# Kernel optimization log

Measured on AMD Instinct MI355X. Metric: run time of the kernel, lower is better.

Reference implementation:

```python
import jax, jax.numpy as jnp
import numpy as np

B, N, F, H = 2, 2048, 1024, 16
D = F // H  # head_dim = 64
SCALE = D ** -0.5


def setup_inputs() -> dict:
    key = jax.random.key(0)
    ks = jax.random.split(key, 5)
    std = F ** -0.5
    return {
        "x": jax.random.normal(ks[0], (B, N, F), dtype=jnp.float32),
        "Wq": jax.random.normal(ks[1], (F, F), dtype=jnp.float32) * std,
        "Wk": jax.random.normal(ks[2], (F, F), dtype=jnp.float32) * std,
        "Wv": jax.random.normal(ks[3], (F, F), dtype=jnp.float32) * std,
        "Wo": jax.random.normal(ks[4], (F, F), dtype=jnp.float32) * std,
        "bo": jnp.zeros((F,), dtype=jnp.float32),
    }


def reference(x, Wq, Wk, Wv, Wo, bo):
    b, n, f = x.shape
    # nn.Linear computes x @ W.T
    q = (x @ Wq.T).reshape(b, n, H, D).transpose(0, 2, 1, 3)  # bhnd
    k = (x @ Wk.T).reshape(b, n, H, D).transpose(0, 2, 1, 3)
    v = (x @ Wv.T).reshape(b, n, H, D).transpose(0, 2, 1, 3)
    score = jax.nn.softmax(jnp.einsum('bhif,bhjf->bhij', q, k) * SCALE, axis=-1)
    attn = jnp.einsum('bhij,bhjf->bihf', score, v)  # (b, n, h, d)
    o = attn.reshape(b, n, f) @ Wo.T + bo
    return o
```

## Files before the change

kernel.cpp:

```cpp
#include <hip/hip_runtime.h>
#include <hip/hip_bf16.h>

#define B_    2
#define NSEQ  2048
#define FDIM  1024
#define NH    16
#define HD    64
#define MTOT  (B_*NSEQ)
#define BHSZ  (NSEQ*HD)

typedef __bf16 bf16_t;
typedef __bf16 bf16x4 __attribute__((ext_vector_type(4)));
typedef __bf16 bf16x8 __attribute__((ext_vector_type(8)));
typedef float  f32x4  __attribute__((ext_vector_type(4)));

#define AS1 __attribute__((address_space(1)))
#define AS3 __attribute__((address_space(3)))

#if __has_builtin(__builtin_amdgcn_exp2f)
#define EXP2(x) __builtin_amdgcn_exp2f(x)
#else
#define EXP2(x) exp2f(x)
#endif

__device__ __forceinline__ void gld_lds16(const bf16_t* g, bf16_t* l) {
  __builtin_amdgcn_global_load_lds((const AS1 void*)g, (AS3 void*)l, 16, 0, 0);
}

extern "C" __global__ __launch_bounds__(256) void cast_all_k(
    const float* __restrict__ x,  const float* __restrict__ wq,
    const float* __restrict__ wk, const float* __restrict__ wv,
    const float* __restrict__ wo,
    bf16_t* __restrict__ xb,  bf16_t* __restrict__ wqb,
    bf16_t* __restrict__ wkb, bf16_t* __restrict__ wvb,
    bf16_t* __restrict__ wob)
{
  long t = (long)blockIdx.x * blockDim.x + threadIdx.x;
  long i = t * 4;
  const float* src; bf16_t* dst; long off;
  if      (i < 4194304L) { src = x;  dst = xb;  off = i; }
  else if (i < 5242880L) { src = wq; dst = wqb; off = i - 4194304L; }
  else if (i < 6291456L) { src = wk; dst = wkb; off = i - 5242880L; }
  else if (i < 7340032L) { src = wv; dst = wvb; off = i - 6291456L; }
  else                   { src = wo; dst = wob; off = i - 7340032L; }
  float4 v = *(const float4*)(src + off);
  bf16x4 o = { (bf16_t)v.x, (bf16_t)v.y, (bf16_t)v.z, (bf16_t)v.w };
  *(bf16x4*)(dst + off) = o;
}

extern "C" __global__ __launch_bounds__(512) void gemm_bt_k(
    const bf16_t* __restrict__ A,
    const bf16_t* __restrict__ Bq, const bf16_t* __restrict__ Bk,
    const bf16_t* __restrict__ Bv,
    bf16_t* __restrict__ oq, bf16_t* __restrict__ okk,
    bf16_t* __restrict__ ovt)
{
  __shared__ __align__(16) char garena[33792];
  bf16_t* As = (bf16_t*)garena;
  bf16_t* Bs = (bf16_t*)(garena + 16384);
  const int K = FDIM;
  int mode = blockIdx.z;
  const bf16_t* Bw = (mode == 0) ? Bq : (mode == 1) ? Bk : Bv;
  int m0 = blockIdx.x * 128, n0 = blockIdx.y * 128;
  int tid = threadIdx.x, lane = tid & 63, wave = tid >> 6;
  int g = lane >> 4, c = lane & 15;
  int wm = (wave & 1) * 64, wn = (wave >> 1) * 32;
  f32x4 acc[4][2];
  for (int i = 0; i < 4; ++i)
    for (int j = 0; j < 2; ++j)
      acc[i][j] = (f32x4){0.f, 0.f, 0.f, 0.f};

  int srow = lane >> 2;
  int scol = (lane & 3) * 8;

  for (int kt = 0; kt < K / 64; ++kt) {
    int kk = kt * 64;
    {
      int chunk = wave;
      const bf16_t* ag = A  + (long)(m0 + chunk*16 + srow) * K + kk + scol;
      const bf16_t* bg = Bw + (long)(n0 + chunk*16 + srow) * K + kk + scol;
      gld_lds16(ag,      As + chunk * 512);
      gld_lds16(ag + 32, As + 4096 + chunk * 512);
      gld_lds16(bg,      Bs + chunk * 512);
      gld_lds16(bg + 32, Bs + 4096 + chunk * 512);
    }
    __syncthreads();
    bf16x8 af[4][2], bfr[2][2];
    for (int t = 0; t < 4; ++t) {
      af[t][0]  = *(const bf16x8*)(As + (wm + t*16 + c) * 32 + g * 8);
      af[t][1]  = *(const bf16x8*)(As + 4096 + (wm + t*16 + c) * 32 + g * 8);
    }
    for (int t = 0; t < 2; ++t) {
      bfr[t][0] = *(const bf16x8*)(Bs + (wn + t*16 + c) * 32 + g * 8);
      bfr[t][1] = *(const bf16x8*)(Bs + 4096 + (wn + t*16 + c) * 32 + g * 8);
    }
    for (int mt = 0; mt < 4; ++mt)
      for (int nt = 0; nt < 2; ++nt) {
        acc[mt][nt] = __builtin_amdgcn_mfma_f32_16x16x32_bf16(
            af[mt][0], bfr[nt][0], acc[mt][nt], 0, 0, 0);
        acc[mt][nt] = __builtin_amdgcn_mfma_f32_16x16x32_bf16(
            af[mt][1], bfr[nt][1], acc[mt][nt], 0, 0, 0);
      }
    __syncthreads();
  }

  bf16_t* Tl = (bf16_t*)garena;
  float sc = (mode == 0) ? 0.18033688011112042f : 1.0f;
  if (mode < 2) {
    for (int mt = 0; mt < 4; ++mt)
      for (int nt = 0; nt < 2; ++nt) {
        int nloc = wn + nt*16 + c;
        for (int r = 0; r < 4; ++r) {
          int mloc = wm + mt*16 + g*4 + r;
          Tl[mloc*132 + nloc] = (bf16_t)(acc[mt][nt][r] * sc);
        }
      }
  } else {
    for (int mt = 0; mt < 4; ++mt)
      for (int nt = 0; nt < 2; ++nt) {
        int nloc = wn + nt*16 + c;
        int mloc = wm + mt*16 + g*4;
        bf16x4 pk = { (bf16_t)acc[mt][nt][0], (bf16_t)acc[mt][nt][1],
                      (bf16_t)acc[mt][nt][2], (bf16_t)acc[mt][nt][3] };
        *(bf16x4*)(Tl + nloc*132 + mloc) = pk;
      }
  }
  __syncthreads();

  int b = m0 >> 11, m0loc = m0 & 2047;
  int h0 = n0 >> 6, tile0 = m0loc >> 6;
  int hoff = (mode == 2) ? 16 : 4;
#pragma unroll
  for (int u = 0; u < 4; ++u) {
    int chunk = u * 512 + tid;
    bf16_t* dst;
    int sidx;
    if (mode == 0) {
      int headloc = chunk >> 10, o = chunk & 1023;
      int tokloc = o >> 3, dd = (o & 7) * 8;
      sidx = tokloc*132 + headloc*64 + dd;
      dst = oq + ((long)(b*NH + h0 + headloc) * NSEQ + m0loc) * HD + (long)o * 8;
    } else if (mode == 1) {
      int region = chunk >> 9, o = chunk & 511;
      int headloc = region >> 1, t = region & 1;
      int f = o >> 6, rest = o & 63;
      int mtA = f >> 1, kh = f & 1, gK = rest >> 4, cA = rest & 15;
      int tokloc = t*64 + mtA*16 + cA;
      sidx = tokloc*132 + headloc*64 + kh*32 + gK*8;
      dst = okk + (long)(b*NH + h0 + headloc) * BHSZ
            + (long)(tile0 + t) * 4096 + (long)o * 8;
    } else {
      int region = chunk >> 9, o = chunk & 511;
      int headloc = region >> 1, t = region & 1;
      int c2 = o >> 8, dt = (o >> 6) & 3, ln = o & 63;
      int gA = ln >> 4, cA = ln & 15;
      sidx = (headloc*64 + dt*16 + cA) * 132 + t*64 + c2*32 + gA*4;
      dst = ovt + (long)(b*NH + h0 + headloc) * BHSZ
            + (long)(tile0 + t) * 4096 + (long)o * 8;
    }
    bf16x4 lo = *(const bf16x4*)(Tl + sidx);
    bf16x4 hi = *(const bf16x4*)(Tl + sidx + hoff);
    bf16x8 v;
#pragma unroll
    for (int i = 0; i < 4; ++i) { v[i] = lo[i]; v[i+4] = hi[i]; }
    *(bf16x8*)dst = v;
  }
}

extern "C" __global__ __launch_bounds__(512) void gemm_out_k(
    const bf16_t* __restrict__ A, const bf16_t* __restrict__ W,
    const float* __restrict__ bias, float* __restrict__ out)
{
  __shared__ __align__(16) bf16_t As[8192];
  __shared__ __align__(16) bf16_t Bs[4096];
  const int K = FDIM;
  int m0 = blockIdx.x * 128, n0 = blockIdx.y * 64;
  int tid = threadIdx.x, lane = tid & 63, wave = tid >> 6;
  int g = lane >> 4, c = lane & 15;
  int wm = (wave & 3) * 32, wn = (wave >> 2) * 32;
  f32x4 acc[2][2];
  for (int i = 0; i < 2; ++i)
    for (int j = 0; j < 2; ++j)
      acc[i][j] = (f32x4){0.f, 0.f, 0.f, 0.f};

  int srow = lane >> 2;
  int scol = (lane & 3) * 8;

  for (int kt = 0; kt < K / 64; ++kt) {
    int kk = kt * 64;
    {
      const bf16_t* ag = A + (long)(m0 + wave*16 + srow) * K + kk + scol;
      gld_lds16(ag,      As + wave * 512);
      gld_lds16(ag + 32, As + 4096 + wave * 512);
      if (wave < 4) {
        const bf16_t* bg = W + (long)(n0 + wave*16 + srow) * K + kk + scol;
        gld_lds16(bg,      Bs + wave * 512);
        gld_lds16(bg + 32, Bs + 2048 + wave * 512);
      }
    }
    __syncthreads();
    bf16x8 af[2][2], bfr[2][2];
    for (int t = 0; t < 2; ++t) {
      af[t][0]  = *(const bf16x8*)(As + (wm + t*16 + c) * 32 + g * 8);
      af[t][1]  = *(const bf16x8*)(As + 4096 + (wm + t*16 + c) * 32 + g * 8);
      bfr[t][0] = *(const bf16x8*)(Bs + (wn + t*16 + c) * 32 + g * 8);
      bfr[t][1] = *(const bf16x8*)(Bs + 2048 + (wn + t*16 + c) * 32 + g * 8);
    }
    for (int mt = 0; mt < 2; ++mt)
      for (int nt = 0; nt < 2; ++nt) {
        acc[mt][nt] = __builtin_amdgcn_mfma_f32_16x16x32_bf16(
            af[mt][0], bfr[nt][0], acc[mt][nt], 0, 0, 0);
        acc[mt][nt] = __builtin_amdgcn_mfma_f32_16x16x32_bf16(
            af[mt][1], bfr[nt][1], acc[mt][nt], 0, 0, 0);
      }
    __syncthreads();
  }

  for (int mt = 0; mt < 2; ++mt)
    for (int nt = 0; nt < 2; ++nt) {
      int n = n0 + wn + nt*16 + c;
      float bv = bias[n];
      for (int r = 0; r < 4; ++r) {
        int m = m0 + wm + mt*16 + g*4 + r;
        out[(long)m * FDIM + n] = acc[mt][nt][r] + bv;
      }
    }
}

extern "C" __global__ __launch_bounds__(512) void attn_fused_k(
    const bf16_t* __restrict__ q, const bf16_t* __restrict__ k,
    const bf16_t* __restrict__ vt, bf16_t* __restrict__ attn)
{
  __shared__ __align__(16) char arena[65536];
  __shared__ float Ll[128];
  int bh = blockIdx.y;
  int tid = threadIdx.x, lane = tid & 63, wave = tid >> 6;
  int g = lane >> 4, c = lane & 15;
  int qg = wave & 3, half = wave >> 2;
  int qw = blockIdx.x * 128 + qg * 32;
  const bf16_t* Q  = q  + (long)bh * NSEQ * HD;
  const bf16_t* Kf = k  + (long)bh * BHSZ;
  const bf16_t* Vf = vt + (long)bh * BHSZ;

  bf16x8 bQ[2][2];
#pragma unroll
  for (int s = 0; s < 2; ++s)
#pragma unroll
    for (int hh = 0; hh < 2; ++hh)
      bQ[s][hh] = *(const bf16x8*)(Q + (long)(qw + s*16 + c) * HD + hh*32 + g*8);

  f32x4 acc[2][4];
  f32x4 accl[2];
#pragma unroll
  for (int s = 0; s < 2; ++s) {
#pragma unroll
    for (int dt = 0; dt < 4; ++dt) acc[s][dt] = (f32x4){0.f, 0.f, 0.f, 0.f};
    accl[s] = (f32x4){0.f, 0.f, 0.f, 0.f};
  }

  bf16x8 ones;
#pragma unroll
  for (int i = 0; i < 8; ++i) ones[i] = (bf16_t)1.0f;

  int w4 = wave & 3, ln = lane;
  const int NT = NSEQ / 128;
  int kbase = half * (NSEQ / 2);

  auto stage = [&](int buf, int k0) {
    bf16_t* Kb = (bf16_t*)(arena + buf * 32768 + half * 16384);
    bf16_t* Vb = Kb + 4096;
    long tbase = (long)(k0 >> 6) * 4096;
#pragma unroll
    for (int j = 0; j < 2; ++j) {
      int ch = j*4 + w4;
      gld_lds16(Kf + tbase + ch*512 + ln*8, Kb + ch*512);
      gld_lds16(Vf + tbase + ch*512 + ln*8, Vb + ch*512);
    }
  };

  stage(0, kbase);
  __syncthreads();

  for (int kt = 0; kt < NT; ++kt) {
    int cur = kt & 1;
    if (kt + 1 < NT) stage(cur ^ 1, kbase + (kt + 1) * 64);

    const bf16_t* Kb = (const bf16_t*)(arena + cur * 32768 + half * 16384);
    const bf16_t* Vb = Kb + 4096;

    f32x4 St[2][4];
    __builtin_amdgcn_s_setprio(1);
#pragma unroll
    for (int mt = 0; mt < 4; ++mt) {
      bf16x8 k0f = *(const bf16x8*)(Kb + (mt*2 + 0) * 512 + lane * 8);
      bf16x8 k1f = *(const bf16x8*)(Kb + (mt*2 + 1) * 512 + lane * 8);
#pragma unroll
      for (int s = 0; s < 2; ++s) {
        f32x4 z = (f32x4){0.f, 0.f, 0.f, 0.f};
        z = __builtin_amdgcn_mfma_f32_16x16x32_bf16(k0f, bQ[s][0], z, 0, 0, 0);
        z = __builtin_amdgcn_mfma_f32_16x16x32_bf16(k1f, bQ[s][1], z, 0, 0, 0);
        St[s][mt] = z;
      }
    }
    __builtin_amdgcn_s_setprio(0);

    bf16x8 bP[2][2];
#pragma unroll
    for (int s = 0; s < 2; ++s)
#pragma unroll
      for (int c2 = 0; c2 < 2; ++c2) {
        f32x4 pa = St[s][c2*2 + 0];
        f32x4 pb = St[s][c2*2 + 1];
        bf16x8 t;
#pragma unroll
        for (int r = 0; r < 4; ++r) {
          t[r]     = (bf16_t)EXP2(pa[r]);
          t[r + 4] = (bf16_t)EXP2(pb[r]);
        }
        bP[s][c2] = t;
      }

    __builtin_amdgcn_s_setprio(1);
#pragma unroll
    for (int c2 = 0; c2 < 2; ++c2) {
      accl[0] = __builtin_amdgcn_mfma_f32_16x16x32_bf16(ones, bP[0][c2], accl[0], 0, 0, 0);
      accl[1] = __builtin_amdgcn_mfma_f32_16x16x32_bf16(ones, bP[1][c2], accl[1], 0, 0, 0);
#pragma unroll
      for (int dt = 0; dt < 4; ++dt) {
        bf16x8 aV = *(const bf16x8*)(Vb + (c2*4 + dt) * 512 + lane * 8);
        acc[0][dt] = __builtin_amdgcn_mfma_f32_16x16x32_bf16(
            aV, bP[0][c2], acc[0][dt], 0, 0, 0);
        acc[1][dt] = __builtin_amdgcn_mfma_f32_16x16x32_bf16(
            aV, bP[1][c2], acc[1][dt], 0, 0, 0);
      }
    }
    __builtin_amdgcn_s_setprio(0);

    __syncthreads();
  }

  float lp[2];
#pragma unroll
  for (int s = 0; s < 2; ++s) lp[s] = accl[s][0];

  float* Opart = (float*)arena;
  bf16_t* Tb = (bf16_t*)(arena + 36864);
  if (half == 1) {
#pragma unroll
    for (int s = 0; s < 2; ++s) {
      int qrow = qg*32 + s*16 + c;
#pragma unroll
      for (int dt = 0; dt < 4; ++dt)
        *(f32x4*)(Opart + qrow*72 + dt*16 + g*4) = acc[s][dt];
      if (g == 0) Ll[qrow] = lp[s];
    }
  }
  __syncthreads();
  if (half == 0) {
#pragma unroll
    for (int s = 0; s < 2; ++s) {
      int qrow = qg*32 + s*16 + c;
      float inv = 1.f / (lp[s] + Ll[qrow]);
#pragma unroll
      for (int dt = 0; dt < 4; ++dt) {
        f32x4 part = *(const f32x4*)(Opart + qrow*72 + dt*16 + g*4);
#pragma unroll
        for (int r = 0; r < 4; ++r)
          Tb[qrow*80 + dt*16 + g*4 + r] =
              (bf16_t)((acc[s][dt][r] + part[r]) * inv);
      }
    }
  }
  __syncthreads();
  int b = bh >> 4, h = bh & 15;
  int row = tid >> 2, dseg = (tid & 3) * 16;
  const bf16_t* src = Tb + row*80 + dseg;
  bf16_t* dst = attn + ((long)(b * NSEQ + blockIdx.x*128 + row)) * FDIM + h * HD + dseg;
  *(bf16x8*)(dst)     = *(const bf16x8*)(src);
  *(bf16x8*)(dst + 8) = *(const bf16x8*)(src + 8);
}

extern "C" void kernel_launch(void* const* d_in, const int* in_sizes, int n_in,
                              void* d_out, int out_size, void* d_ws, size_t ws_size,
                              hipStream_t stream)
{
  const float* x  = (const float*)d_in[0];
  const float* wq = (const float*)d_in[1];
  const float* wk = (const float*)d_in[2];
  const float* wv = (const float*)d_in[3];
  const float* wo = (const float*)d_in[4];
  const float* bo = (const float*)d_in[5];
  float* out = (float*)d_out;
  char* ws = (char*)d_ws;

  const size_t MB = 1024 * 1024;
  bf16_t* xb    = (bf16_t*)(ws);
  bf16_t* wqb   = (bf16_t*)(ws + 8  * MB);
  bf16_t* wkb   = (bf16_t*)(ws + 10 * MB);
  bf16_t* wvb   = (bf16_t*)(ws + 12 * MB);
  bf16_t* wob   = (bf16_t*)(ws + 14 * MB);
  bf16_t* q_ws  = (bf16_t*)(ws + 16 * MB);
  bf16_t* k_ws  = (bf16_t*)(ws + 24 * MB);
  bf16_t* vt_ws = (bf16_t*)(ws + 32 * MB);
  bf16_t* at_ws = (bf16_t*)(ws + 40 * MB);

  hipLaunchKernelGGL(cast_all_k, dim3(8192), dim3(256), 0, stream,
                     x, wq, wk, wv, wo, xb, wqb, wkb, wvb, wob);

  hipLaunchKernelGGL(gemm_bt_k, dim3(32, 8, 3), dim3(512), 0, stream,
                     xb, wqb, wkb, wvb, q_ws, k_ws, vt_ws);

  hipLaunchKernelGGL(attn_fused_k, dim3(16, 32), dim3(512), 0, stream,
                     q_ws, k_ws, vt_ws, at_ws);

  hipLaunchKernelGGL(gemm_out_k, dim3(32, 16), dim3(512), 0, stream,
                     at_ws, wob, bo, out);
}
```

Before: 166.9 us.

## Fuse Q/K/V projections into one block sharing the A tile

The QKV projection kernel now computes all three outputs (Q, K, V) in one block instead of launching a z-dimension of three. Each block loads the x tile once and reuses it against three weight tiles, which removes the repeated A loads and LDS fragment reads. In exchange the block uses 64KB of LDS and three times the accumulator registers, and the grid shrinks from 768 to 256 blocks. That lowers occupancy and could leave CUs underused.

```diff
diff --git a/kernel.cpp b/kernel.cpp
--- a/kernel.cpp
+++ b/kernel.cpp
@@ -48,27 +48,26 @@
   *(bf16x4*)(dst + off) = o;
 }
 
-extern "C" __global__ __launch_bounds__(512) void gemm_bt_k(
+extern "C" __global__ __launch_bounds__(512) void gemm_qkv_k(
     const bf16_t* __restrict__ A,
     const bf16_t* __restrict__ Bq, const bf16_t* __restrict__ Bk,
     const bf16_t* __restrict__ Bv,
     bf16_t* __restrict__ oq, bf16_t* __restrict__ okk,
     bf16_t* __restrict__ ovt)
 {
-  __shared__ __align__(16) char garena[33792];
+  __shared__ __align__(16) char garena[65536];
   bf16_t* As = (bf16_t*)garena;
-  bf16_t* Bs = (bf16_t*)(garena + 16384);
   const int K = FDIM;
-  int mode = blockIdx.z;
-  const bf16_t* Bw = (mode == 0) ? Bq : (mode == 1) ? Bk : Bv;
   int m0 = blockIdx.x * 128, n0 = blockIdx.y * 128;
   int tid = threadIdx.x, lane = tid & 63, wave = tid >> 6;
   int g = lane >> 4, c = lane & 15;
   int wm = (wave & 1) * 64, wn = (wave >> 1) * 32;
-  f32x4 acc[4][2];
-  for (int i = 0; i < 4; ++i)
-    for (int j = 0; j < 2; ++j)
-      acc[i][j] = (f32x4){0.f, 0.f, 0.f, 0.f};
+  f32x4 acc[3][4][2];
+#pragma unroll
+  for (int m = 0; m < 3; ++m)
+    for (int i = 0; i < 4; ++i)
+      for (int j = 0; j < 2; ++j)
+        acc[m][i][j] = (f32x4){0.f, 0.f, 0.f, 0.f};
 
   int srow = lane >> 2;
   int scol = (lane & 3) * 8;
@@ -76,94 +75,121 @@
   for (int kt = 0; kt < K / 64; ++kt) {
     int kk = kt * 64;
     {
-      int chunk = wave;
-      const bf16_t* ag = A  + (long)(m0 + chunk*16 + srow) * K + kk + scol;
-      const bf16_t* bg = Bw + (long)(n0 + chunk*16 + srow) * K + kk + scol;
-      gld_lds16(ag,      As + chunk * 512);
-      gld_lds16(ag + 32, As + 4096 + chunk * 512);
-      gld_lds16(bg,      Bs + chunk * 512);
-      gld_lds16(bg + 32, Bs + 4096 + chunk * 512);
-    }
-    __syncthreads();
-    bf16x8 af[4][2], bfr[2][2];
+      long rowoff = (long)(wave*16 + srow) * K + kk + scol;
+      const bf16_t* ag = A  + (long)m0 * K + rowoff;
+      const bf16_t* q0 = Bq + (long)n0 * K + rowoff;
+      const bf16_t* k0 = Bk + (long)n0 * K + rowoff;
+      const bf16_t* v0 = Bv + (long)n0 * K + rowoff;
+      bf16_t* Bs0 = (bf16_t*)(garena + 16384);
+      bf16_t* Bs1 = (bf16_t*)(garena + 32768);
+      bf16_t* Bs2 = (bf16_t*)(garena + 49152);
+      gld_lds16(ag,      As  + wave * 512);
+      gld_lds16(ag + 32, As  + 4096 + wave * 512);
+      gld_lds16(q0,      Bs0 + wave * 512);
+      gld_lds16(q0 + 32, Bs0 + 4096 + wave * 512);
+      gld_lds16(k0,      Bs1 + wave * 512);
+      gld_lds16(k0 + 32, Bs1 + 4096 + wave * 512);
+      gld_lds16(v0,      Bs2 + wave * 512);
+      gld_lds16(v0 + 32, Bs2 + 4096 + wave * 512);
+    }
+    __syncthreads();
+    bf16x8 af[4][2];
+#pragma unroll
     for (int t = 0; t < 4; ++t) {
-      af[t][0]  = *(const bf16x8*)(As + (wm + t*16 + c) * 32 + g * 8);
-      af[t][1]  = *(const bf16x8*)(As + 4096 + (wm + t*16 + c) * 32 + g * 8);
-    }
-    for (int t = 0; t < 2; ++t) {
-      bfr[t][0] = *(const bf16x8*)(Bs + (wn + t*16 + c) * 32 + g * 8);
-      bfr[t][1] = *(const bf16x8*)(Bs + 4096 + (wn + t*16 + c) * 32 + g * 8);
-    }
-    for (int mt = 0; mt < 4; ++mt)
-      for (int nt = 0; nt < 2; ++nt) {
-        acc[mt][nt] = __builtin_amdgcn_mfma_f32_16x16x32_bf16(
-            af[mt][0], bfr[nt][0], acc[mt][nt], 0, 0, 0);
-        acc[mt][nt] = __builtin_amdgcn_mfma_f32_16x16x32_bf16(
-            af[mt][1], bfr[nt][1], acc[mt][nt], 0, 0, 0);
-      }
+      af[t][0] = *(const bf16x8*)(As + (wm + t*16 + c) * 32 + g * 8);
+      af[t][1] = *(const bf16x8*)(As + 4096 + (wm + t*16 + c) * 32 + g * 8);
+    }
+#pragma unroll
+    for (int md = 0; md < 3; ++md) {
+      const bf16_t* Bs = (const bf16_t*)(garena + 16384 + md * 16384);
+      bf16x8 bfr[2][2];
+#pragma unroll
+      for (int t = 0; t < 2; ++t) {
+        bfr[t][0] = *(const bf16x8*)(Bs + (wn + t*16 + c) * 32 + g * 8);
+        bfr[t][1] = *(const bf16x8*)(Bs + 4096 + (wn + t*16 + c) * 32 + g * 8);
+      }
+#pragma unroll
+      for (int mt = 0; mt < 4; ++mt)
+#pragma unroll
+        for (int nt = 0; nt < 2; ++nt) {
+          acc[md][mt][nt] = __builtin_amdgcn_mfma_f32_16x16x32_bf16(
+              af[mt][0], bfr[nt][0], acc[md][mt][nt], 0, 0, 0);
+          acc[md][mt][nt] = __builtin_amdgcn_mfma_f32_16x16x32_bf16(
+              af[mt][1], bfr[nt][1], acc[md][mt][nt], 0, 0, 0);
+        }
+    }
     __syncthreads();
   }
 
   bf16_t* Tl = (bf16_t*)garena;
-  float sc = (mode == 0) ? 0.18033688011112042f : 1.0f;
-  if (mode < 2) {
-    for (int mt = 0; mt < 4; ++mt)
-      for (int nt = 0; nt < 2; ++nt) {
-        int nloc = wn + nt*16 + c;
-        for (int r = 0; r < 4; ++r) {
-          int mloc = wm + mt*16 + g*4 + r;
-          Tl[mloc*132 + nloc] = (bf16_t)(acc[mt][nt][r] * sc);
-        }
-      }
-  } else {
-    for (int mt = 0; mt < 4; ++mt)
-      for (int nt = 0; nt < 2; ++nt) {
-        int nloc = wn + nt*16 + c;
-        int mloc = wm + mt*16 + g*4;
-        bf16x4 pk = { (bf16_t)acc[mt][nt][0], (bf16_t)acc[mt][nt][1],
-                      (bf16_t)acc[mt][nt][2], (bf16_t)acc[mt][nt][3] };
-        *(bf16x4*)(Tl + nloc*132 + mloc) = pk;
-      }
-  }
-  __syncthreads();
-
   int b = m0 >> 11, m0loc = m0 & 2047;
   int h0 = n0 >> 6, tile0 = m0loc >> 6;
-  int hoff = (mode == 2) ? 16 : 4;
-#pragma unroll
-  for (int u = 0; u < 4; ++u) {
-    int chunk = u * 512 + tid;
-    bf16_t* dst;
-    int sidx;
-    if (mode == 0) {
-      int headloc = chunk >> 10, o = chunk & 1023;
-      int tokloc = o >> 3, dd = (o & 7) * 8;
-      sidx = tokloc*132 + headloc*64 + dd;
-      dst = oq + ((long)(b*NH + h0 + headloc) * NSEQ + m0loc) * HD + (long)o * 8;
-    } else if (mode == 1) {
-      int region = chunk >> 9, o = chunk & 511;
-      int headloc = region >> 1, t = region & 1;
-      int f = o >> 6, rest = o & 63;
-      int mtA = f >> 1, kh = f & 1, gK = rest >> 4, cA = rest & 15;
-      int tokloc = t*64 + mtA*16 + cA;
-      sidx = tokloc*132 + headloc*64 + kh*32 + gK*8;
-      dst = okk + (long)(b*NH + h0 + headloc) * BHSZ
-            + (long)(tile0 + t) * 4096 + (long)o * 8;
+#pragma unroll
+  for (int mode = 0; mode < 3; ++mode) {
+    float sc = (mode == 0) ? 0.18033688011112042f : 1.0f;
+    if (mode < 2) {
+#pragma unroll
+      for (int mt = 0; mt < 4; ++mt)
+#pragma unroll
+        for (int nt = 0; nt < 2; ++nt) {
+          int nloc = wn + nt*16 + c;
+#pragma unroll
+          for (int r = 0; r < 4; ++r) {
+            int mloc = wm + mt*16 + g*4 + r;
+            Tl[mloc*132 + nloc] = (bf16_t)(acc[mode][mt][nt][r] * sc);
+          }
+        }
     } else {
-      int region = chunk >> 9, o = chunk & 511;
-      int headloc = region >> 1, t = region & 1;
-      int c2 = o >> 8, dt = (o >> 6) & 3, ln = o & 63;
-      int gA = ln >> 4, cA = ln & 15;
-      sidx = (headloc*64 + dt*16 + cA) * 132 + t*64 + c2*32 + gA*4;
-      dst = ovt + (long)(b*NH + h0 + headloc) * BHSZ
-            + (long)(tile0 + t) * 4096 + (long)o * 8;
-    }
-    bf16x4 lo = *(const bf16x4*)(Tl + sidx);
-    bf16x4 hi = *(const bf16x4*)(Tl + sidx + hoff);
-    bf16x8 v;
-#pragma unroll
-    for (int i = 0; i < 4; ++i) { v[i] = lo[i]; v[i+4] = hi[i]; }
-    *(bf16x8*)dst = v;
+#pragma unroll
+      for (int mt = 0; mt < 4; ++mt)
+#pragma unroll
+        for (int nt = 0; nt < 2; ++nt) {
+          int nloc = wn + nt*16 + c;
+          int mloc = wm + mt*16 + g*4;
+          bf16x4 pk = { (bf16_t)acc[mode][mt][nt][0], (bf16_t)acc[mode][mt][nt][1],
+                        (bf16_t)acc[mode][mt][nt][2], (bf16_t)acc[mode][mt][nt][3] };
+          *(bf16x4*)(Tl + nloc*132 + mloc) = pk;
+        }
+    }
+    __syncthreads();
+
+    int hoff = (mode == 2) ? 16 : 4;
+#pragma unroll
+    for (int u = 0; u < 4; ++u) {
+      int chunk = u * 512 + tid;
+      bf16_t* dst;
+      int sidx;
+      if (mode == 0) {
+        int headloc = chunk >> 10, o = chunk & 1023;
+        int tokloc = o >> 3, dd = (o & 7) * 8;
+        sidx = tokloc*132 + headloc*64 + dd;
+        dst = oq + ((long)(b*NH + h0 + headloc) * NSEQ + m0loc) * HD + (long)o * 8;
+      } else if (mode == 1) {
+        int region = chunk >> 9, o = chunk & 511;
+        int headloc = region >> 1, t = region & 1;
+        int f = o >> 6, rest = o & 63;
+        int mtA = f >> 1, kh = f & 1, gK = rest >> 4, cA = rest & 15;
+        int tokloc = t*64 + mtA*16 + cA;
+        sidx = tokloc*132 + headloc*64 + kh*32 + gK*8;
+        dst = okk + (long)(b*NH + h0 + headloc) * BHSZ
+              + (long)(tile0 + t) * 4096 + (long)o * 8;
+      } else {
+        int region = chunk >> 9, o = chunk & 511;
+        int headloc = region >> 1, t = region & 1;
+        int c2 = o >> 8, dt = (o >> 6) & 3, ln = o & 63;
+        int gA = ln >> 4, cA = ln & 15;
+        sidx = (headloc*64 + dt*16 + cA) * 132 + t*64 + c2*32 + gA*4;
+        dst = ovt + (long)(b*NH + h0 + headloc) * BHSZ
+              + (long)(tile0 + t) * 4096 + (long)o * 8;
+      }
+      bf16x4 lo = *(const bf16x4*)(Tl + sidx);
+      bf16x4 hi = *(const bf16x4*)(Tl + sidx + hoff);
+      bf16x8 v;
+#pragma unroll
+      for (int i = 0; i < 4; ++i) { v[i] = lo[i]; v[i+4] = hi[i]; }
+      *(bf16x8*)dst = v;
+    }
+    __syncthreads();
   }
 }
 
@@ -407,7 +433,7 @@
   hipLaunchKernelGGL(cast_all_k, dim3(8192), dim3(256), 0, stream,
                      x, wq, wk, wv, wo, xb, wqb, wkb, wvb, wob);
 
-  hipLaunchKernelGGL(gemm_bt_k, dim3(32, 8, 3), dim3(512), 0, stream,
+  hipLaunchKernelGGL(gemm_qkv_k, dim3(32, 8), dim3(512), 0, stream,
                      xb, wqb, wkb, wvb, q_ws, k_ws, vt_ws);
 
   hipLaunchKernelGGL(attn_fused_k, dim3(16, 32), dim3(512), 0, stream,
```

New measurement: 177.6 us. +6.4%, slower.

## Double K-tile depth in output GEMM with XOR-swizzled LDS layout

Applied to the files above, without the earlier changes.

The output-projection GEMM now stages 128-wide K tiles instead of 64, halving the number of barrier-separated loop iterations. Each lane loads a full row segment of 128 elements into LDS using an XOR swizzle on the 16-byte chunk index to avoid bank conflicts, and reads fragments with the matching swizzle. LDS usage doubles, which may reduce occupancy. This GEMM is only one of several kernels, so its effect on total time is limited.

```diff
diff --git a/kernel.cpp b/kernel.cpp
--- a/kernel.cpp
+++ b/kernel.cpp
@@ -171,8 +171,8 @@
     const bf16_t* __restrict__ A, const bf16_t* __restrict__ W,
     const float* __restrict__ bias, float* __restrict__ out)
 {
-  __shared__ __align__(16) bf16_t As[8192];
-  __shared__ __align__(16) bf16_t Bs[4096];
+  __shared__ __align__(16) bf16_t As[16384];
+  __shared__ __align__(16) bf16_t Bs[8192];
   const int K = FDIM;
   int m0 = blockIdx.x * 128, n0 = blockIdx.y * 64;
   int tid = threadIdx.x, lane = tid & 63, wave = tid >> 6;
@@ -183,36 +183,46 @@
     for (int j = 0; j < 2; ++j)
       acc[i][j] = (f32x4){0.f, 0.f, 0.f, 0.f};
 
-  int srow = lane >> 2;
-  int scol = (lane & 3) * 8;
-
-  for (int kt = 0; kt < K / 64; ++kt) {
-    int kk = kt * 64;
+  int srow = lane >> 4;
+  int sgrp = (lane & 15) ^ (srow << 2);
+  int scol = sgrp * 8;
+
+  for (int kt = 0; kt < K / 128; ++kt) {
+    int kk = kt * 128;
     {
-      const bf16_t* ag = A + (long)(m0 + wave*16 + srow) * K + kk + scol;
-      gld_lds16(ag,      As + wave * 512);
-      gld_lds16(ag + 32, As + 4096 + wave * 512);
-      if (wave < 4) {
-        const bf16_t* bg = W + (long)(n0 + wave*16 + srow) * K + kk + scol;
-        gld_lds16(bg,      Bs + wave * 512);
-        gld_lds16(bg + 32, Bs + 2048 + wave * 512);
+#pragma unroll
+      for (int j = 0; j < 4; ++j) {
+        int ch = wave * 4 + j;
+        const bf16_t* ag = A + (long)(m0 + ch*4 + srow) * K + kk + scol;
+        gld_lds16(ag, As + ch * 512);
+      }
+#pragma unroll
+      for (int j = 0; j < 2; ++j) {
+        int ch = wave * 2 + j;
+        const bf16_t* bg = W + (long)(n0 + ch*4 + srow) * K + kk + scol;
+        gld_lds16(bg, Bs + ch * 512);
       }
     }
     __syncthreads();
-    bf16x8 af[2][2], bfr[2][2];
-    for (int t = 0; t < 2; ++t) {
-      af[t][0]  = *(const bf16x8*)(As + (wm + t*16 + c) * 32 + g * 8);
-      af[t][1]  = *(const bf16x8*)(As + 4096 + (wm + t*16 + c) * 32 + g * 8);
-      bfr[t][0] = *(const bf16x8*)(Bs + (wn + t*16 + c) * 32 + g * 8);
-      bfr[t][1] = *(const bf16x8*)(Bs + 2048 + (wn + t*16 + c) * 32 + g * 8);
-    }
-    for (int mt = 0; mt < 2; ++mt)
-      for (int nt = 0; nt < 2; ++nt) {
-        acc[mt][nt] = __builtin_amdgcn_mfma_f32_16x16x32_bf16(
-            af[mt][0], bfr[nt][0], acc[mt][nt], 0, 0, 0);
-        acc[mt][nt] = __builtin_amdgcn_mfma_f32_16x16x32_bf16(
-            af[mt][1], bfr[nt][1], acc[mt][nt], 0, 0, 0);
-      }
+#pragma unroll
+    for (int kh = 0; kh < 4; ++kh) {
+      bf16x8 af[2], bfr[2];
+#pragma unroll
+      for (int t = 0; t < 2; ++t) {
+        int ar = wm + t*16 + c;
+        af[t]  = *(const bf16x8*)(As + (ar>>2)*512 + (ar&3)*128
+                                     + ((kh ^ (ar&3))*4 + g)*8);
+        int br = wn + t*16 + c;
+        bfr[t] = *(const bf16x8*)(Bs + (br>>2)*512 + (br&3)*128
+                                     + ((kh ^ (br&3))*4 + g)*8);
+      }
+#pragma unroll
+      for (int mt = 0; mt < 2; ++mt)
+#pragma unroll
+        for (int nt = 0; nt < 2; ++nt)
+          acc[mt][nt] = __builtin_amdgcn_mfma_f32_16x16x32_bf16(
+              af[mt], bfr[nt], acc[mt][nt], 0, 0, 0);
+    }
     __syncthreads();
   }
 
```

Measured after the change: 168.8 us. About the same (+1.1%).
